# Optimization experiments

Measured on AMD Instinct MI355X. Metric: run time of the kernel, lower is better.

Reference implementation:

```python
import jax, jax.numpy as jnp
import numpy as np

N = 100000      # nodes
E = 1600000     # edges
F_IN = 512      # num_node_features
HID = 128       # hidden_dim (GCN2Conv channels)
C = 64          # num_classes
L = 8           # n_layers
ALPHA = 0.1
THETA = 0.5


def setup_inputs() -> dict:
    key = jax.random.key(0)
    ks = jax.random.split(key, 7)
    x = jax.random.normal(ks[0], (N, F_IN), jnp.float32)
    edge_index = jax.random.randint(ks[1], (2, E), 0, N, dtype=jnp.int64)
    # fcs[0]: Linear(F_IN, HID); stored as [in, out] so forward is x @ w + b
    w_in = jax.random.normal(ks[2], (F_IN, HID), jnp.float32) / np.sqrt(F_IN)
    b_in = jnp.zeros((HID,), jnp.float32)
    # one shared [H, H] weight per GCN2Conv layer (shared_weights=True)
    conv_w = jax.random.normal(ks[3], (L, HID, HID), jnp.float32) / np.sqrt(HID)
    # fcs[-1]: Linear(HID, C)
    w_out = jax.random.normal(ks[4], (HID, C), jnp.float32) / np.sqrt(HID)
    b_out = jnp.zeros((C,), jnp.float32)
    return dict(x=x, edge_index=edge_index, w_in=w_in, b_in=b_in,
                conv_w=conv_w, w_out=w_out, b_out=b_out)


def _gcn_norm(edge_index, num_nodes):
    # PyG gcn_norm with add_self_loops=True, edge_weight=1
    loops = jnp.arange(num_nodes, dtype=edge_index.dtype)
    src = jnp.concatenate([edge_index[0], loops])
    dst = jnp.concatenate([edge_index[1], loops])
    deg = jax.ops.segment_sum(jnp.ones_like(dst, jnp.float32), dst,
                              num_segments=num_nodes)
    dinv = jnp.where(deg > 0, jax.lax.rsqrt(jnp.maximum(deg, 1e-12)), 0.0)
    norm = dinv[src] * dinv[dst]  # [E + N]
    return src, dst, norm


def reference(x, edge_index, w_in, b_in, conv_w, w_out, b_out):
    src, dst, norm = _gcn_norm(edge_index, N)
    h = x @ w_in + b_in          # fcs[0]; [N, HID]
    h0 = h                       # initial residual
    for l in range(L):
        beta = float(np.log(THETA / (l + 1) + 1.0))
        # sparse neighbor aggregation: out[i] = sum_e norm[e] * h[src[e]]
        agg = jax.ops.segment_sum(h[src] * norm[:, None], dst, num_segments=N)
        s = (1.0 - ALPHA) * agg + ALPHA * h0           # initial residual mix
        h = jax.nn.elu((1.0 - beta) * s + beta * (s @ conv_w[l]))  # identity mapping
        # dropout omitted (eval mode / training=False)
    logits = h @ w_out + b_out   # fcs[-1]
    return jax.nn.log_softmax(logits, axis=-1)
```

## Files before the change

kernel.cpp:

```cpp
#include <hip/hip_runtime.h>
#include <math.h>

#define N_NODES 100000
#define N_EDGES 1600000
#define F_IN    512
#define HID     128
#define NCLS    64
#define NLAYERS 8
#define NT      (N_NODES / 16)
#define NSCANB  ((N_NODES + 255) / 256)

typedef __attribute__((ext_vector_type(8))) short short8;
typedef __attribute__((ext_vector_type(4))) float float4v;

#define SWZB(b) ((b) ^ ((((b) >> 8) & 3) << 4))

__device__ inline unsigned short f2bf(float f) {
    unsigned int u = __float_as_uint(f);
    unsigned int r = u + 0x7fffu + ((u >> 16) & 1u);
    return (unsigned short)(r >> 16);
}
__device__ inline float bf2f(unsigned short h) {
    return __uint_as_float(((unsigned int)h) << 16);
}
__device__ inline uint4 pack8(const unsigned short* v) {
    uint4 u;
    u.x = (unsigned)v[0] | ((unsigned)v[1] << 16);
    u.y = (unsigned)v[2] | ((unsigned)v[3] << 16);
    u.z = (unsigned)v[4] | ((unsigned)v[5] << 16);
    u.w = (unsigned)v[6] | ((unsigned)v[7] << 16);
    return u;
}
__device__ inline void bf8_fma(float* a, uint4 u, float v) {
    a[0] += v * __uint_as_float(u.x << 16);
    a[1] += v * __uint_as_float(u.x & 0xffff0000u);
    a[2] += v * __uint_as_float(u.y << 16);
    a[3] += v * __uint_as_float(u.y & 0xffff0000u);
    a[4] += v * __uint_as_float(u.z << 16);
    a[5] += v * __uint_as_float(u.z & 0xffff0000u);
    a[6] += v * __uint_as_float(u.w << 16);
    a[7] += v * __uint_as_float(u.w & 0xffff0000u);
}
__device__ inline void unpack8(float* f, uint4 u) {
    f[0] = __uint_as_float(u.x << 16); f[1] = __uint_as_float(u.x & 0xffff0000u);
    f[2] = __uint_as_float(u.y << 16); f[3] = __uint_as_float(u.y & 0xffff0000u);
    f[4] = __uint_as_float(u.z << 16); f[5] = __uint_as_float(u.z & 0xffff0000u);
    f[6] = __uint_as_float(u.w << 16); f[7] = __uint_as_float(u.w & 0xffff0000u);
}
__device__ inline void split_into(short8& ahi, short8& alo, int j, float f) {
    unsigned short h = f2bf(f);
    ahi[j] = (short)h;
    alo[j] = (short)f2bf(f - bf2f(h));
}


__global__ __launch_bounds__(256) void cnt_init(int* __restrict__ cnt) {
    int i = blockIdx.x * 256 + threadIdx.x;
    if (i < N_NODES) cnt[i] = 0;
}
__global__ __launch_bounds__(256) void cnt_count(const int* __restrict__ dst,
                                                 int* __restrict__ cnt) {
    int e = blockIdx.x * 256 + threadIdx.x;
    if (e < N_EDGES) atomicAdd(&cnt[dst[e]], 1);
}
__global__ __launch_bounds__(256) void make_dinv(const int* __restrict__ cnt,
                                                 float* __restrict__ dinv) {
    int i = blockIdx.x * 256 + threadIdx.x;
    if (i < N_NODES) dinv[i] = rsqrtf((float)(cnt[i] + 1));
}
__global__ __launch_bounds__(256) void scan_block(const int* __restrict__ cnt,
                                                  int* __restrict__ partial,
                                                  int* __restrict__ bsum) {
    __shared__ int tmp[256];
    int t = threadIdx.x, i = blockIdx.x * 256 + t;
    int v = (i < N_NODES) ? cnt[i] : 0;
    tmp[t] = v;
    __syncthreads();
#pragma unroll
    for (int off = 1; off < 256; off <<= 1) {
        int add = (t >= off) ? tmp[t - off] : 0;
        __syncthreads();
        tmp[t] += add;
        __syncthreads();
    }
    if (i < N_NODES) partial[i] = tmp[t];
    if (t == 255) bsum[blockIdx.x] = tmp[255];
}
__global__ void scan_bsum(int* __restrict__ bsum) {
    if (threadIdx.x == 0 && blockIdx.x == 0) {
        int acc = 0;
        for (int i = 0; i < NSCANB; i++) { int v = bsum[i]; bsum[i] = acc; acc += v; }
    }
}
__global__ __launch_bounds__(256) void finalize_rowptr(const int* __restrict__ cnt,
                                                       const int* __restrict__ partial,
                                                       const int* __restrict__ bsum,
                                                       int* __restrict__ row_ptr,
                                                       int* __restrict__ cursor) {
    int i = blockIdx.x * 256 + threadIdx.x;
    if (i < N_NODES) {
        int ex = partial[i] - cnt[i] + bsum[blockIdx.x];
        row_ptr[i] = ex;
        cursor[i]  = ex;
        if (i == N_NODES - 1) row_ptr[N_NODES] = ex + cnt[i];
    }
}
__global__ __launch_bounds__(256) void scatter_edges(const int* __restrict__ srcI,
                                                     const int* __restrict__ dstI,
                                                     const float* __restrict__ dinv,
                                                     int* __restrict__ cursor,
                                                     int2* __restrict__ rec) {
    int e = blockIdx.x * 256 + threadIdx.x;
    if (e < N_EDGES) {
        int s = srcI[e], d = dstI[e];
        int pos = atomicAdd(&cursor[d], 1);
        rec[pos] = make_int2(s, __float_as_int(dinv[s] * dinv[d]));
    }
}

__global__ __launch_bounds__(64) void conv_win(const float* __restrict__ w,
                                               unsigned short* __restrict__ wip) {
    int nt = blockIdx.x >> 4;
    int c  = blockIdx.x & 15;
    int lane = threadIdx.x;
    int n  = nt * 16 + (lane & 15);
    int kb = c * 32 + (lane >> 4) * 8;
    unsigned short hi[8], lo[8];
#pragma unroll
    for (int j = 0; j < 8; j++) {
        float v = w[(size_t)(kb + j) * HID + n];
        hi[j] = f2bf(v);
        lo[j] = f2bf(v - bf2f(hi[j]));
    }
    size_t base = ((size_t)c * 8 + nt) * 1024 + (size_t)lane * 8;
    *(uint4*)&wip[base]       = pack8(hi);
    *(uint4*)&wip[base + 512] = pack8(lo);
}

__global__ __launch_bounds__(64) void conv_wl(const float* __restrict__ cw,
                                              unsigned short* __restrict__ wlp) {
    int l  = blockIdx.x >> 5;
    int nt = (blockIdx.x >> 2) & 7;
    int c  = blockIdx.x & 3;
    int lane = threadIdx.x;
    float beta = logf(0.5f / (float)(l + 1) + 1.0f);
    int n  = nt * 16 + (lane & 15);
    int kb = c * 32 + (lane >> 4) * 8;
    const float* W = cw + (size_t)l * HID * HID;
    unsigned short hi[8], lo[8];
#pragma unroll
    for (int j = 0; j < 8; j++) {
        int k = kb + j;
        float v = beta * W[(size_t)k * HID + n] + ((k == n) ? (1.0f - beta) : 0.0f);
        hi[j] = f2bf(v);
        lo[j] = f2bf(v - bf2f(hi[j]));
    }
    size_t base = (size_t)l * 32768 + ((size_t)c * 8 + nt) * 1024 + (size_t)lane * 8;
    *(uint4*)&wlp[base]       = pack8(hi);
    *(uint4*)&wlp[base + 512] = pack8(lo);
}

__global__ __launch_bounds__(64) void conv_wout(const float* __restrict__ w,
                                                unsigned short* __restrict__ wop) {
    int nt = blockIdx.x >> 2;
    int c  = blockIdx.x & 3;
    int lane = threadIdx.x;
    int n  = nt * 16 + (lane & 15);
    int kb = c * 32 + (lane >> 4) * 8;
    unsigned short hi[8], lo[8];
#pragma unroll
    for (int j = 0; j < 8; j++) {
        float v = w[(size_t)(kb + j) * NCLS + n];
        hi[j] = f2bf(v);
        lo[j] = f2bf(v - bf2f(hi[j]));
    }
    size_t base = ((size_t)nt * 4 + c) * 1024 + (size_t)lane * 8;
    *(uint4*)&wop[base]       = pack8(hi);
    *(uint4*)&wop[base + 512] = pack8(lo);
}

__global__ __launch_bounds__(256) void in_gemm_mfma(const float* __restrict__ x,
        const unsigned short* __restrict__ wip, const float* __restrict__ bias,
        unsigned short* __restrict__ hb, unsigned short* __restrict__ h0b) {
    __shared__ unsigned short wlds[8192];
    __shared__ unsigned short tile[64][136];
    int tid = threadIdx.x;
    int wave = tid >> 6, lane = tid & 63;
    int t = blockIdx.x * 4 + wave;
    int m = lane & 15, q = lane >> 4;
    int tc = (t < NT) ? t : (NT - 1);

    const uint4* wg = (const uint4*)wip;
    uint4 pf0 = wg[tid];
    uint4 pf1 = wg[tid + 256];
    uint4 pf2 = wg[tid + 512];
    uint4 pf3 = wg[tid + 768];

    float4v acc[8];
#pragma unroll
    for (int nt = 0; nt < 8; nt++) acc[nt] = (float4v){0.f, 0.f, 0.f, 0.f};
    const float* xr = x + (size_t)(tc * 16 + m) * F_IN + q * 8;
    uint4* wl4 = (uint4*)wlds;

    for (int c = 0; c < 16; c++) {
        wl4[tid] = pf0; wl4[tid + 256] = pf1; wl4[tid + 512] = pf2; wl4[tid + 768] = pf3;
        __syncthreads();
        if (c < 15) {
            const uint4* wn = wg + (size_t)(c + 1) * 1024;
            pf0 = wn[tid]; pf1 = wn[tid + 256]; pf2 = wn[tid + 512]; pf3 = wn[tid + 768];
        }
        float4 x0 = *(const float4*)(xr + c * 32);
        float4 x1 = *(const float4*)(xr + c * 32 + 4);
        short8 ahi, alo;
        split_into(ahi, alo, 0, x0.x); split_into(ahi, alo, 1, x0.y);
        split_into(ahi, alo, 2, x0.z); split_into(ahi, alo, 3, x0.w);
        split_into(ahi, alo, 4, x1.x); split_into(ahi, alo, 5, x1.y);
        split_into(ahi, alo, 6, x1.z); split_into(ahi, alo, 7, x1.w);
#pragma unroll
        for (int nt = 0; nt < 8; nt++) {
            short8 bhi = *(short8*)&wlds[nt * 1024 + lane * 8];
            short8 blo = *(short8*)&wlds[nt * 1024 + 512 + lane * 8];
            acc[nt] = __builtin_amdgcn_mfma_f32_16x16x32_bf16(ahi, bhi, acc[nt], 0, 0, 0);
            acc[nt] = __builtin_amdgcn_mfma_f32_16x16x32_bf16(ahi, blo, acc[nt], 0, 0, 0);
            acc[nt] = __builtin_amdgcn_mfma_f32_16x16x32_bf16(alo, bhi, acc[nt], 0, 0, 0);
        }
        __syncthreads();
    }

    if (t < NT) {
#pragma unroll
        for (int nt = 0; nt < 8; nt++) {
            float bb = bias[nt * 16 + m];
#pragma unroll
            for (int r = 0; r < 4; r++)
                tile[wave * 16 + q * 4 + r][nt * 16 + m] = f2bf(acc[nt][r] + bb);
        }
    }
    __syncthreads();

    int nl = tid >> 2, part = tid & 3;
    int node = blockIdx.x * 64 + nl;
    if (node < N_NODES) {
        uint4* d1 = (uint4*)&hb [(size_t)node * HID + part * 32];
        uint4* d2 = (uint4*)&h0b[(size_t)node * HID + part * 32];
#pragma unroll
        for (int j = 0; j < 4; j++) {
            uint4 u = *(uint4*)&tile[nl][part * 32 + j * 8];
            d1[j] = u; d2[j] = u;
        }
    }
}

template <int LAST>
__global__ __launch_bounds__(256, 4) void spmm_gemm(const int* __restrict__ row_ptr,
        const int2* __restrict__ rec, const float* __restrict__ dinv,
        const unsigned short* __restrict__ hin, const unsigned short* __restrict__ h0b,
        const unsigned short* __restrict__ wlp, void* __restrict__ outp) {
    __shared__ __align__(16) unsigned short afr[16384];
    int tid = threadIdx.x;
    int wave = tid >> 6, lane = tid & 63;
    int qu = lane >> 4, fl = lane & 15;
    char* af = (char*)afr;

    int base = blockIdx.x * 64 + wave * 16;
#pragma unroll 1
    for (int g = 0; g < 4; ++g) {
        int node = base + g * 4 + qu;
        int nc = (node < N_NODES) ? node : (N_NODES - 1);
        int e0 = row_ptr[nc], e1 = row_ptr[nc + 1];
        float dd = dinv[nc];
        uint4 hv = *(const uint4*)(hin + (size_t)nc * HID + fl * 8);
        uint4 zv = *(const uint4*)(h0b + (size_t)nc * HID + fl * 8);
        float a[8] = {0.f, 0.f, 0.f, 0.f, 0.f, 0.f, 0.f, 0.f};
        int e = e0;
        for (; e + 7 < e1; e += 8) {
            int2 r0 = rec[e],     r1 = rec[e + 1], r2 = rec[e + 2], r3 = rec[e + 3];
            int2 r4 = rec[e + 4], r5 = rec[e + 5], r6 = rec[e + 6], r7 = rec[e + 7];
            uint4 u0 = *(const uint4*)(hin + (size_t)r0.x * HID + fl * 8);
            uint4 u1 = *(const uint4*)(hin + (size_t)r1.x * HID + fl * 8);
            uint4 u2 = *(const uint4*)(hin + (size_t)r2.x * HID + fl * 8);
            uint4 u3 = *(const uint4*)(hin + (size_t)r3.x * HID + fl * 8);
            uint4 u4 = *(const uint4*)(hin + (size_t)r4.x * HID + fl * 8);
            uint4 u5 = *(const uint4*)(hin + (size_t)r5.x * HID + fl * 8);
            uint4 u6 = *(const uint4*)(hin + (size_t)r6.x * HID + fl * 8);
            uint4 u7 = *(const uint4*)(hin + (size_t)r7.x * HID + fl * 8);
            bf8_fma(a, u0, __int_as_float(r0.y));
            bf8_fma(a, u1, __int_as_float(r1.y));
            bf8_fma(a, u2, __int_as_float(r2.y));
            bf8_fma(a, u3, __int_as_float(r3.y));
            bf8_fma(a, u4, __int_as_float(r4.y));
            bf8_fma(a, u5, __int_as_float(r5.y));
            bf8_fma(a, u6, __int_as_float(r6.y));
            bf8_fma(a, u7, __int_as_float(r7.y));
        }
        for (; e + 3 < e1; e += 4) {
            int2 r0 = rec[e], r1 = rec[e + 1], r2 = rec[e + 2], r3 = rec[e + 3];
            uint4 u0 = *(const uint4*)(hin + (size_t)r0.x * HID + fl * 8);
            uint4 u1 = *(const uint4*)(hin + (size_t)r1.x * HID + fl * 8);
            uint4 u2 = *(const uint4*)(hin + (size_t)r2.x * HID + fl * 8);
            uint4 u3 = *(const uint4*)(hin + (size_t)r3.x * HID + fl * 8);
            bf8_fma(a, u0, __int_as_float(r0.y));
            bf8_fma(a, u1, __int_as_float(r1.y));
            bf8_fma(a, u2, __int_as_float(r2.y));
            bf8_fma(a, u3, __int_as_float(r3.y));
        }
        for (; e < e1; ++e) {
            int2 r0 = rec[e];
            uint4 u0 = *(const uint4*)(hin + (size_t)r0.x * HID + fl * 8);
            bf8_fma(a, u0, __int_as_float(r0.y));
        }
        float d2 = dd * dd;
        float hvf[8], zvf[8];
        unpack8(hvf, hv);
        unpack8(zvf, zv);
        short8 ohi, olo;
#pragma unroll
        for (int j = 0; j < 8; ++j) {
            float o = 0.9f * (a[j] + d2 * hvf[j]) + 0.1f * zvf[j];
            split_into(ohi, olo, j, o);
        }
        int mrow = g * 4 + qu;
        int b0 = wave * 8192 + (fl >> 2) * 2048 + (fl & 3) * 256 + mrow * 16;
        *(short8*)(af + SWZB(b0)) = ohi;
        *(short8*)(af + SWZB(b0 + 1024)) = olo;
    }
    __syncthreads();

    float4v acc[8];
#pragma unroll
    for (int nt = 0; nt < 8; ++nt) acc[nt] = (float4v){0.f, 0.f, 0.f, 0.f};
    const short8* wp8 = (const short8*)wlp;
#pragma unroll
    for (int c = 0; c < 4; ++c) {
        int rb = wave * 8192 + c * 2048 + lane * 16;
        short8 ahi = *(const short8*)(af + SWZB(rb));
        short8 alo = *(const short8*)(af + SWZB(rb + 1024));
#pragma unroll
        for (int nt = 0; nt < 8; ++nt) {
            short8 bhi = wp8[(size_t)(c * 8 + nt) * 128 + lane];
            short8 blo = wp8[(size_t)(c * 8 + nt) * 128 + 64 + lane];
            acc[nt] = __builtin_amdgcn_mfma_f32_16x16x32_bf16(ahi, bhi, acc[nt], 0, 0, 0);
            acc[nt] = __builtin_amdgcn_mfma_f32_16x16x32_bf16(ahi, blo, acc[nt], 0, 0, 0);
            acc[nt] = __builtin_amdgcn_mfma_f32_16x16x32_bf16(alo, bhi, acc[nt], 0, 0, 0);
        }
    }

    if (LAST) {
        int t = blockIdx.x * 4 + wave;
        if (t < NT) {
            float* hf = (float*)outp;
#pragma unroll
            for (int nt = 0; nt < 8; ++nt) {
#pragma unroll
                for (int r = 0; r < 4; ++r) {
                    float v = acc[nt][r];
                    v = (v > 0.f) ? v : (expf(v) - 1.0f);
                    hf[(size_t)(t * 16 + qu * 4 + r) * HID + nt * 16 + fl] = v;
                }
            }
        }
    } else {
        __syncthreads();
        unsigned short (*tile)[136] = (unsigned short (*)[136])afr;
#pragma unroll
        for (int nt = 0; nt < 8; ++nt) {
#pragma unroll
            for (int r = 0; r < 4; ++r) {
                float v = acc[nt][r];
                v = (v > 0.f) ? v : (expf(v) - 1.0f);
                tile[wave * 16 + qu * 4 + r][nt * 16 + fl] = f2bf(v);
            }
        }
        __syncthreads();
        unsigned short* hout = (unsigned short*)outp;
        int nl = tid >> 2, part = tid & 3;
        int node = blockIdx.x * 64 + nl;
        if (node < N_NODES) {
            uint4* d1 = (uint4*)&hout[(size_t)node * HID + part * 32];
#pragma unroll
            for (int j = 0; j < 4; ++j) d1[j] = *(uint4*)&tile[nl][part * 32 + j * 8];
        }
    }
}

__global__ __launch_bounds__(256) void out_gemm(const float* __restrict__ hf,
        const unsigned short* __restrict__ wop, const float* __restrict__ bias,
        float* __restrict__ out) {
    int wave = threadIdx.x >> 6;
    int lane = threadIdx.x & 63;
    int t = blockIdx.x * 4 + wave;
    int m = lane & 15, q = lane >> 4;
    if (t >= NT) return;

    float4v acc[4];
#pragma unroll
    for (int nt = 0; nt < 4; nt++) acc[nt] = (float4v){0.f, 0.f, 0.f, 0.f};
    const float* hr = hf + (size_t)(t * 16 + m) * HID + q * 8;
    const short8* wp8 = (const short8*)wop;
#pragma unroll
    for (int c = 0; c < 4; c++) {
        float4 x0 = *(const float4*)(hr + c * 32);
        float4 x1 = *(const float4*)(hr + c * 32 + 4);
        short8 ahi, alo;
        split_into(ahi, alo, 0, x0.x); split_into(ahi, alo, 1, x0.y);
        split_into(ahi, alo, 2, x0.z); split_into(ahi, alo, 3, x0.w);
        split_into(ahi, alo, 4, x1.x); split_into(ahi, alo, 5, x1.y);
        split_into(ahi, alo, 6, x1.z); split_into(ahi, alo, 7, x1.w);
#pragma unroll
        for (int nt = 0; nt < 4; nt++) {
            short8 bhi = wp8[(size_t)(nt * 4 + c) * 128 + lane];
            short8 blo = wp8[(size_t)(nt * 4 + c) * 128 + 64 + lane];
            acc[nt] = __builtin_amdgcn_mfma_f32_16x16x32_bf16(ahi, bhi, acc[nt], 0, 0, 0);
            acc[nt] = __builtin_amdgcn_mfma_f32_16x16x32_bf16(ahi, blo, acc[nt], 0, 0, 0);
            acc[nt] = __builtin_amdgcn_mfma_f32_16x16x32_bf16(alo, bhi, acc[nt], 0, 0, 0);
        }
    }
    float bn[4];
#pragma unroll
    for (int nt = 0; nt < 4; nt++) bn[nt] = bias[nt * 16 + m];
#pragma unroll
    for (int r = 0; r < 4; r++) {
        float v0 = acc[0][r] + bn[0], v1 = acc[1][r] + bn[1];
        float v2 = acc[2][r] + bn[2], v3 = acc[3][r] + bn[3];
        float mx = fmaxf(fmaxf(v0, v1), fmaxf(v2, v3));
#pragma unroll
        for (int msk = 1; msk < 16; msk <<= 1) mx = fmaxf(mx, __shfl_xor(mx, msk));
        float ssum = expf(v0 - mx) + expf(v1 - mx) + expf(v2 - mx) + expf(v3 - mx);
#pragma unroll
        for (int msk = 1; msk < 16; msk <<= 1) ssum += __shfl_xor(ssum, msk);
        float lg = mx + logf(ssum);
        size_t base = (size_t)(t * 16 + q * 4 + r) * NCLS + m;
        out[base]      = v0 - lg;
        out[base + 16] = v1 - lg;
        out[base + 32] = v2 - lg;
        out[base + 48] = v3 - lg;
    }
}


extern "C" void kernel_launch(void* const* d_in, const int* in_sizes, int n_in,
                              void* d_out, int out_size, void* d_ws, size_t ws_size,
                              hipStream_t stream) {
    const float* x      = (const float*)d_in[0];
    const int*   ei     = (const int*)  d_in[1];
    const float* w_in   = (const float*)d_in[2];
    const float* b_in   = (const float*)d_in[3];
    const float* conv_w = (const float*)d_in[4];
    const float* w_out  = (const float*)d_in[5];
    const float* b_out  = (const float*)d_in[6];
    float* out = (float*)d_out;

    const int* srcI = ei;
    const int* dstI = ei + N_EDGES;

    char* ws = (char*)d_ws;
    float* dinv    = (float*)(ws + 0x000000);
    int*   cnt     = (int*)  (ws + 0x080000);
    int*   partial = (int*)  (ws + 0x100000);
    int*   bsum    = (int*)  (ws + 0x180000);
    int*   row_ptr = (int*)  (ws + 0x190000);
    int*   cursor  = (int*)  (ws + 0x200000);
    int2*  rec     = (int2*) (ws + 0x280000);
    unsigned short* wip = (unsigned short*)(ws + 0xF00000);
    unsigned short* wlp = (unsigned short*)(ws + 0xF40000);
    unsigned short* wop = (unsigned short*)(ws + 0xFC0000);
    unsigned short* hb  = (unsigned short*)(ws + 0x1000000);
    unsigned short* h0b = hb + (size_t)N_NODES * HID;
    unsigned short* hb2 = h0b + (size_t)N_NODES * HID;
    float* hf = (float*)(hb2 + 2 * (size_t)N_NODES * HID);

    int gN = (N_NODES + 255) / 256;
    int gE = (N_EDGES + 255) / 256;
    int gT = (NT + 3) / 4;

    cnt_init<<<gN, 256, 0, stream>>>(cnt);
    cnt_count<<<gE, 256, 0, stream>>>(dstI, cnt);
    make_dinv<<<gN, 256, 0, stream>>>(cnt, dinv);
    scan_block<<<NSCANB, 256, 0, stream>>>(cnt, partial, bsum);
    scan_bsum<<<1, 64, 0, stream>>>(bsum);
    finalize_rowptr<<<NSCANB, 256, 0, stream>>>(cnt, partial, bsum, row_ptr, cursor);
    scatter_edges<<<gE, 256, 0, stream>>>(srcI, dstI, dinv, cursor, rec);

    conv_win<<<128, 64, 0, stream>>>(w_in, wip);
    conv_wl<<<256, 64, 0, stream>>>(conv_w, wlp);
    conv_wout<<<16, 64, 0, stream>>>(w_out, wop);

    in_gemm_mfma<<<gT, 256, 0, stream>>>(x, wip, b_in, hb, h0b);

    unsigned short* cur = hb;
    unsigned short* nxt = hb2;
    for (int l = 0; l < NLAYERS; l++) {
        const unsigned short* wl = wlp + (size_t)l * 32768;
        if (l < NLAYERS - 1) {
            spmm_gemm<0><<<gT, 256, 0, stream>>>(row_ptr, rec, dinv, cur, h0b, wl, nxt);
            unsigned short* t = cur; cur = nxt; nxt = t;
        } else {
            spmm_gemm<1><<<gT, 256, 0, stream>>>(row_ptr, rec, dinv, cur, h0b, wl, hf);
        }
    }

    out_gemm<<<gT, 256, 0, stream>>>(hf, wop, b_out, out);
}
```

Before: 1.208 ms.

## Fuse output linear and log-softmax into last layer; parallelize block-sum scan

The final layer's activations are no longer written to global memory as fp32 for a separate out_gemm kernel. They are split into bf16 hi/lo parts in shared memory, and the output GEMM, bias and log-softmax run in the same kernel. The serial single-thread scan of block sums is also replaced with a 256-thread parallel scan. This removes an N x 128 fp32 round trip through global memory, one kernel launch, and a serial loop, at the cost of more shared-memory traffic and registers in the last layer's kernel.

```diff
diff --git a/kernel.cpp b/kernel.cpp
--- a/kernel.cpp
+++ b/kernel.cpp
@@ -14,6 +14,7 @@
 typedef __attribute__((ext_vector_type(4))) float float4v;
 
 #define SWZB(b) ((b) ^ ((((b) >> 8) & 3) << 4))
+#define SWZC(b) ((b) ^ ((((b) >> 8) & 7) << 4))
 
 __device__ inline unsigned short f2bf(float f) {
     unsigned int u = __float_as_uint(f);
@@ -86,11 +87,25 @@
     if (i < N_NODES) partial[i] = tmp[t];
     if (t == 255) bsum[blockIdx.x] = tmp[255];
 }
-__global__ void scan_bsum(int* __restrict__ bsum) {
-    if (threadIdx.x == 0 && blockIdx.x == 0) {
-        int acc = 0;
-        for (int i = 0; i < NSCANB; i++) { int v = bsum[i]; bsum[i] = acc; acc += v; }
-    }
+__global__ __launch_bounds__(256) void scan_b2(int* __restrict__ b) {
+    __shared__ int ps[256];
+    int t = threadIdx.x;
+    int i0 = 2 * t, i1 = 2 * t + 1;
+    int v0 = (i0 < NSCANB) ? b[i0] : 0;
+    int v1 = (i1 < NSCANB) ? b[i1] : 0;
+    int s = v0 + v1;
+    ps[t] = s;
+    __syncthreads();
+#pragma unroll
+    for (int off = 1; off < 256; off <<= 1) {
+        int add = (t >= off) ? ps[t - off] : 0;
+        __syncthreads();
+        ps[t] += add;
+        __syncthreads();
+    }
+    int excl = ps[t] - s;
+    if (i0 < NSCANB) b[i0] = excl;
+    if (i1 < NSCANB) b[i1] = excl + v0;
 }
 __global__ __launch_bounds__(256) void finalize_rowptr(const int* __restrict__ cnt,
                                                        const int* __restrict__ partial,
@@ -255,7 +270,8 @@
 __global__ __launch_bounds__(256, 4) void spmm_gemm(const int* __restrict__ row_ptr,
         const int2* __restrict__ rec, const float* __restrict__ dinv,
         const unsigned short* __restrict__ hin, const unsigned short* __restrict__ h0b,
-        const unsigned short* __restrict__ wlp, void* __restrict__ outp) {
+        const unsigned short* __restrict__ wlp, const unsigned short* __restrict__ wop,
+        const float* __restrict__ obias, void* __restrict__ outp) {
     __shared__ __align__(16) unsigned short afr[16384];
     int tid = threadIdx.x;
     int wave = tid >> 6, lane = tid & 63;
@@ -347,16 +363,63 @@
 
     if (LAST) {
         int t = blockIdx.x * 4 + wave;
+        __syncthreads();
+        char* wb = af + wave * 8192;
         if (t < NT) {
-            float* hf = (float*)outp;
 #pragma unroll
             for (int nt = 0; nt < 8; ++nt) {
 #pragma unroll
                 for (int r = 0; r < 4; ++r) {
                     float v = acc[nt][r];
                     v = (v > 0.f) ? v : (expf(v) - 1.0f);
-                    hf[(size_t)(t * 16 + qu * 4 + r) * HID + nt * 16 + fl] = v;
+                    unsigned short h = f2bf(v);
+                    unsigned short l = f2bf(v - bf2f(h));
+                    int b = (qu * 4 + r) * 256 + (nt * 16 + fl) * 2;
+                    *(unsigned short*)(wb + SWZC(b)) = h;
+                    *(unsigned short*)(wb + 4096 + SWZC(b)) = l;
                 }
+            }
+        }
+        __syncthreads();
+        if (t < NT) {
+            float4v oc[4];
+#pragma unroll
+            for (int nt = 0; nt < 4; ++nt) oc[nt] = (float4v){0.f, 0.f, 0.f, 0.f};
+            const short8* wq = (const short8*)wop;
+#pragma unroll
+            for (int c = 0; c < 4; ++c) {
+                int rb = fl * 256 + (c * 32 + qu * 8) * 2;
+                short8 ahi = *(const short8*)(wb + SWZC(rb));
+                short8 alo = *(const short8*)(wb + 4096 + SWZC(rb));
+#pragma unroll
+                for (int nt = 0; nt < 4; ++nt) {
+                    short8 bhi = wq[(size_t)(nt * 4 + c) * 128 + lane];
+                    short8 blo = wq[(size_t)(nt * 4 + c) * 128 + 64 + lane];
+                    oc[nt] = __builtin_amdgcn_mfma_f32_16x16x32_bf16(ahi, bhi, oc[nt], 0, 0, 0);
+                    oc[nt] = __builtin_amdgcn_mfma_f32_16x16x32_bf16(ahi, blo, oc[nt], 0, 0, 0);
+                    oc[nt] = __builtin_amdgcn_mfma_f32_16x16x32_bf16(alo, bhi, oc[nt], 0, 0, 0);
+                }
+            }
+            float* out = (float*)outp;
+            float bn[4];
+#pragma unroll
+            for (int nt = 0; nt < 4; ++nt) bn[nt] = obias[nt * 16 + fl];
+#pragma unroll
+            for (int r = 0; r < 4; ++r) {
+                float v0 = oc[0][r] + bn[0], v1 = oc[1][r] + bn[1];
+                float v2 = oc[2][r] + bn[2], v3 = oc[3][r] + bn[3];
+                float mx = fmaxf(fmaxf(v0, v1), fmaxf(v2, v3));
+#pragma unroll
+                for (int msk = 1; msk < 16; msk <<= 1) mx = fmaxf(mx, __shfl_xor(mx, msk));
+                float ssum = expf(v0 - mx) + expf(v1 - mx) + expf(v2 - mx) + expf(v3 - mx);
+#pragma unroll
+                for (int msk = 1; msk < 16; msk <<= 1) ssum += __shfl_xor(ssum, msk);
+                float lg = mx + logf(ssum);
+                size_t ob = (size_t)(t * 16 + qu * 4 + r) * NCLS + fl;
+                out[ob]      = v0 - lg;
+                out[ob + 16] = v1 - lg;
+                out[ob + 32] = v2 - lg;
+                out[ob + 48] = v3 - lg;
             }
         }
     } else {
@@ -380,60 +443,6 @@
 #pragma unroll
             for (int j = 0; j < 4; ++j) d1[j] = *(uint4*)&tile[nl][part * 32 + j * 8];
         }
-    }
-}
-
-__global__ __launch_bounds__(256) void out_gemm(const float* __restrict__ hf,
-        const unsigned short* __restrict__ wop, const float* __restrict__ bias,
-        float* __restrict__ out) {
-    int wave = threadIdx.x >> 6;
-    int lane = threadIdx.x & 63;
-    int t = blockIdx.x * 4 + wave;
-    int m = lane & 15, q = lane >> 4;
-    if (t >= NT) return;
-
-    float4v acc[4];
-#pragma unroll
-    for (int nt = 0; nt < 4; nt++) acc[nt] = (float4v){0.f, 0.f, 0.f, 0.f};
-    const float* hr = hf + (size_t)(t * 16 + m) * HID + q * 8;
-    const short8* wp8 = (const short8*)wop;
-#pragma unroll
-    for (int c = 0; c < 4; c++) {
-        float4 x0 = *(const float4*)(hr + c * 32);
-        float4 x1 = *(const float4*)(hr + c * 32 + 4);
-        short8 ahi, alo;
-        split_into(ahi, alo, 0, x0.x); split_into(ahi, alo, 1, x0.y);
-        split_into(ahi, alo, 2, x0.z); split_into(ahi, alo, 3, x0.w);
-        split_into(ahi, alo, 4, x1.x); split_into(ahi, alo, 5, x1.y);
-        split_into(ahi, alo, 6, x1.z); split_into(ahi, alo, 7, x1.w);
-#pragma unroll
-        for (int nt = 0; nt < 4; nt++) {
-            short8 bhi = wp8[(size_t)(nt * 4 + c) * 128 + lane];
-            short8 blo = wp8[(size_t)(nt * 4 + c) * 128 + 64 + lane];
-            acc[nt] = __builtin_amdgcn_mfma_f32_16x16x32_bf16(ahi, bhi, acc[nt], 0, 0, 0);
-            acc[nt] = __builtin_amdgcn_mfma_f32_16x16x32_bf16(ahi, blo, acc[nt], 0, 0, 0);
-            acc[nt] = __builtin_amdgcn_mfma_f32_16x16x32_bf16(alo, bhi, acc[nt], 0, 0, 0);
-        }
-    }
-    float bn[4];
-#pragma unroll
-    for (int nt = 0; nt < 4; nt++) bn[nt] = bias[nt * 16 + m];
-#pragma unroll
-    for (int r = 0; r < 4; r++) {
-        float v0 = acc[0][r] + bn[0], v1 = acc[1][r] + bn[1];
-        float v2 = acc[2][r] + bn[2], v3 = acc[3][r] + bn[3];
-        float mx = fmaxf(fmaxf(v0, v1), fmaxf(v2, v3));
-#pragma unroll
-        for (int msk = 1; msk < 16; msk <<= 1) mx = fmaxf(mx, __shfl_xor(mx, msk));
-        float ssum = expf(v0 - mx) + expf(v1 - mx) + expf(v2 - mx) + expf(v3 - mx);
-#pragma unroll
-        for (int msk = 1; msk < 16; msk <<= 1) ssum += __shfl_xor(ssum, msk);
-        float lg = mx + logf(ssum);
-        size_t base = (size_t)(t * 16 + q * 4 + r) * NCLS + m;
-        out[base]      = v0 - lg;
-        out[base + 16] = v1 - lg;
-        out[base + 32] = v2 - lg;
-        out[base + 48] = v3 - lg;
     }
 }
 
@@ -467,7 +476,6 @@
     unsigned short* hb  = (unsigned short*)(ws + 0x1000000);
     unsigned short* h0b = hb + (size_t)N_NODES * HID;
     unsigned short* hb2 = h0b + (size_t)N_NODES * HID;
-    float* hf = (float*)(hb2 + 2 * (size_t)N_NODES * HID);
 
     int gN = (N_NODES + 255) / 256;
     int gE = (N_EDGES + 255) / 256;
@@ -477,7 +485,7 @@
     cnt_count<<<gE, 256, 0, stream>>>(dstI, cnt);
     make_dinv<<<gN, 256, 0, stream>>>(cnt, dinv);
     scan_block<<<NSCANB, 256, 0, stream>>>(cnt, partial, bsum);
-    scan_bsum<<<1, 64, 0, stream>>>(bsum);
+    scan_b2<<<1, 256, 0, stream>>>(bsum);
     finalize_rowptr<<<NSCANB, 256, 0, stream>>>(cnt, partial, bsum, row_ptr, cursor);
     scatter_edges<<<gE, 256, 0, stream>>>(srcI, dstI, dinv, cursor, rec);
 
@@ -492,12 +500,12 @@
     for (int l = 0; l < NLAYERS; l++) {
         const unsigned short* wl = wlp + (size_t)l * 32768;
         if (l < NLAYERS - 1) {
-            spmm_gemm<0><<<gT, 256, 0, stream>>>(row_ptr, rec, dinv, cur, h0b, wl, nxt);
+            spmm_gemm<0><<<gT, 256, 0, stream>>>(row_ptr, rec, dinv, cur, h0b, wl,
+                                                 nullptr, nullptr, nxt);
             unsigned short* t = cur; cur = nxt; nxt = t;
         } else {
-            spmm_gemm<1><<<gT, 256, 0, stream>>>(row_ptr, rec, dinv, cur, h0b, wl, hf);
-        }
-    }
-
-    out_gemm<<<gT, 256, 0, stream>>>(hf, wop, b_out, out);
-}
+            spmm_gemm<1><<<gT, 256, 0, stream>>>(row_ptr, rec, dinv, cur, h0b, wl,
+                                                 wop, b_out, out);
+        }
+    }
+}
```

New measurement: 1.189 ms. Within noise of the previous version (-1.6%).
